# Optimization experiments

Hardware: AMD Instinct MI355X
Metric: run time of the kernel (lower is better)

Reference implementation:

```python
import jax, jax.numpy as jnp
import numpy as np

PARAM = 10.0
EPS = 1e-10

def delu(x):
    # delu_feature_map: param*relu(x) + (exp(param*min(x,0)) - 1) + 1
    return PARAM * jax.nn.relu(x) + jnp.expm1(PARAM * jnp.minimum(x, 0.0)) + 1.0

def conv1x1(x, w, b):
    # x: (B,C,H,W), w: (O,C), b: (O,)
    return jnp.einsum('oc,bchw->bohw', w, x) + b[None, :, None, None]

def conv3x3(x, w, b):
    # x: (B,C,H,W), w: (O,C,3,3)
    y = jax.lax.conv_general_dilated(x, w, window_strides=(1, 1), padding='SAME',
                                     dimension_numbers=('NCHW', 'OIHW', 'NCHW'))
    return y + b[None, :, None, None]

def setup_inputs() -> dict:
    key = jax.random.key(0)
    B, C, H, W = 4, 256, 128, 128
    ks = jax.random.split(key, 20)
    s = 0.05
    d = {
        'x1': jax.random.normal(ks[0], (B, C, H, W), jnp.float32),
        'x2': jax.random.normal(ks[1], (B, C, H, W), jnp.float32),
        'wq1': jax.random.normal(ks[2], (C, C), jnp.float32) * s,
        'bq1': jax.random.normal(ks[3], (C,), jnp.float32) * s,
        'wk1': jax.random.normal(ks[4], (C, C), jnp.float32) * s,
        'bk1': jax.random.normal(ks[5], (C,), jnp.float32) * s,
        'wv1': jax.random.normal(ks[6], (C, C), jnp.float32) * s,
        'bv1': jax.random.normal(ks[7], (C,), jnp.float32) * s,
        'wq2': jax.random.normal(ks[8], (C, C), jnp.float32) * s,
        'bq2': jax.random.normal(ks[9], (C,), jnp.float32) * s,
        'wk2': jax.random.normal(ks[10], (C, C), jnp.float32) * s,
        'bk2': jax.random.normal(ks[11], (C,), jnp.float32) * s,
        'wv2': jax.random.normal(ks[12], (C, C), jnp.float32) * s,
        'bv2': jax.random.normal(ks[13], (C,), jnp.float32) * s,
        'wd1': jax.random.normal(ks[14], (C, C), jnp.float32) * s,
        'bd1': jax.random.normal(ks[15], (C,), jnp.float32) * s,
        'wd3': jax.random.normal(ks[16], (C, C, 3, 3), jnp.float32) * s,
        'bd3': jax.random.normal(ks[17], (C,), jnp.float32) * s,
        'gamma1': jax.random.normal(ks[18], (1,), jnp.float32) * 0.5,
        'gamma2': jax.random.normal(ks[19], (1,), jnp.float32) * 0.5,
    }
    return d

def reference(x1, x2, wq1, bq1, wk1, bk1, wv1, bv1, wq2, bq2, wk2, bk2,
              wv2, bv2, wd1, bd1, wd3, bd3, gamma1, gamma2):
    B, C, H, W = x1.shape
    N = H * W
    # QKV projections (1x1 convs), flattened to (B,C,N). delu is elementwise,
    # so applying it on (B,C,N) equals the permute/delu/permute in torch.
    q1 = delu(conv1x1(x1, wq1, bq1).reshape(B, C, N))
    k1 = delu(conv1x1(x1, wk1, bk1).reshape(B, C, N))
    v1 = conv1x1(x1, wv1, bv1).reshape(B, C, N)
    q2 = delu(conv1x1(x2, wq2, bq2).reshape(B, C, N))
    k2 = delu(conv1x1(x2, wk2, bk2).reshape(B, C, N))
    v2 = conv1x1(x2, wv2, bv2).reshape(B, C, N)

    # energy: (B,C,C) cross-kernel matrices
    energy1 = jnp.einsum('bmn,bcn->bmc', q1, k2)
    energy2 = jnp.einsum('bmn,bcn->bmc', q2, k1)

    KV1 = k1 * v1  # (B,C,N)
    KV2 = k2 * v2

    # norm: 1 / (sum_{m,c} energy[b,m,c] * k[b,c,n] + eps) -> (B,N)
    esum1 = energy1.sum(axis=1)  # (B,C)
    esum2 = energy2.sum(axis=1)
    norm1 = 1.0 / (jnp.einsum('bc,bcn->bn', esum1, k2) + EPS)
    norm2 = 1.0 / (jnp.einsum('bc,bcn->bn', esum2, k1) + EPS)

    # einsum('bmc,bcn,bn->bcn') factorizes: sum over m hits only energy
    att1 = (esum1[:, :, None] * KV1 * norm1[:, None, :]).reshape(B, C, H, W)
    att2 = (esum2[:, :, None] * KV2 * norm2[:, None, :]).reshape(B, C, H, W)

    out1 = att1 + conv1x1(x1, wd1, bd1) + conv3x3(x1, wd3, bd3)
    out2 = att2 + conv1x1(x2, wd1, bd1) + conv3x3(x2, wd3, bd3)
    out1 = x1 + gamma1[0] * out1
    out2 = x2 + gamma2[0] * out2
    return (out1, out2)
```

## Files before the change

### kernel.cpp

```cpp
#include <hip/hip_runtime.h>
#include <stdint.h>

#define Bn 4
#define Cn 256
#define Hn 128
#define Wn 128
#define Nn 16384
#define EPSn 1e-10f

typedef unsigned short u16;
typedef __attribute__((ext_vector_type(8))) short short8;
typedef __attribute__((ext_vector_type(4))) short short4v;
typedef __attribute__((ext_vector_type(4))) float f32x4;

#define GLOAD_LDS16(g, l)                                                        \
    __builtin_amdgcn_global_load_lds(                                            \
        (const __attribute__((address_space(1))) unsigned int*)(const void*)(g), \
        (__attribute__((address_space(3))) unsigned int*)(void*)(l), 16, 0, 0)

#define MFMA16(a, b, c) __builtin_amdgcn_mfma_f32_16x16x32_bf16(a, b, c, 0, 0, 0)

__device__ __forceinline__ float bf2f(u16 u) {
    union { float f; uint32_t i; } v; v.i = ((uint32_t)u) << 16; return v.f;
}
__device__ __forceinline__ u16 f2bf(float f) {
    union { float f; uint32_t i; } v; v.f = f;
    uint32_t r = v.i + 0x7FFFu + ((v.i >> 16) & 1u);
    return (u16)(r >> 16);
}
__device__ __forceinline__ float delu_f(float x) {
    return x >= 0.f ? fmaf(10.f, x, 1.f) : __expf(10.f * x);
}

__global__ void prep_kernel(const float* __restrict__ wq1, const float* __restrict__ wk1,
                            const float* __restrict__ wv1,
                            const float* __restrict__ wq2, const float* __restrict__ wk2,
                            const float* __restrict__ wv2,
                            const float* __restrict__ wd1, const float* __restrict__ wd3,
                            const float* __restrict__ bd1, const float* __restrict__ bd3,
                            const float* __restrict__ gamma1, const float* __restrict__ gamma2,
                            u16* __restrict__ wq1p, u16* __restrict__ wk1p, u16* __restrict__ wv1p,
                            u16* __restrict__ wq2p, u16* __restrict__ wk2p, u16* __restrict__ wv2p,
                            u16* __restrict__ wallp1, u16* __restrict__ wallp2,
                            float* __restrict__ bfused)
{
    int idx = blockIdx.x * 256 + threadIdx.x;
    int o = idx >> 8, c = idx & 255;
    if (idx < 256) bfused[idx] = bd1[idx] + bd3[idx];
    int s = o >> 6, mf = (o >> 4) & 3, lr = o & 15;
    int kc = c >> 5, lk = (c >> 3) & 3, j = c & 7;
    int poff = ((kc * 4 + s) * 4 + mf) * 512 + (lk * 16 + lr) * 8 + j;
    wq1p[poff] = f2bf(wq1[idx]);
    wk1p[poff] = f2bf(wk1[idx]);
    wv1p[poff] = f2bf(wv1[idx]);
    wq2p[poff] = f2bf(wq2[idx]);
    wk2p[poff] = f2bf(wk2[idx]);
    wv2p[poff] = f2bf(wv2[idx]);
    float wd1v = wd1[idx];
    float inv1 = 1.f / gamma1[0];
    float inv2 = 1.f / gamma2[0];
    float diag = (o == c) ? 1.f : 0.f;
    #pragma unroll
    for (int tap = 0; tap < 9; ++tap) {
        float w = wd3[idx * 9 + tap] + (tap == 4 ? wd1v : 0.f);
        wallp1[tap * 65536 + poff] = f2bf(w + (tap == 4 ? diag * inv1 : 0.f));
        wallp2[tap * 65536 + poff] = f2bf(w + (tap == 4 ? diag * inv2 : 0.f));
    }
}

__global__ void transpose_kernel(const float* __restrict__ x, u16* __restrict__ xT)
{
    __shared__ __align__(16) u16 tl[64][72];
    int t = threadIdx.x;
    int n0 = blockIdx.x * 64, c0 = blockIdx.y * 64, b = blockIdx.z;
    int cl = t >> 4, nl = (t & 15) * 4;
    #pragma unroll
    for (int pc = 0; pc < 4; ++pc) {
        int c = pc * 16 + cl;
        float4 v = *(const float4*)&x[((size_t)(b * Cn + c0 + c)) * Nn + n0 + nl];
        tl[nl + 0][c] = f2bf(v.x);
        tl[nl + 1][c] = f2bf(v.y);
        tl[nl + 2][c] = f2bf(v.z);
        tl[nl + 3][c] = f2bf(v.w);
    }
    __syncthreads();
    #pragma unroll
    for (int ps = 0; ps < 2; ++ps) {
        int id = ps * 256 + t;
        int nr = id >> 3, cc = (id & 7) * 8;
        short8 v = *(const short8*)&tl[nr][cc];
        *(short8*)&xT[((size_t)(b * Nn + n0 + nr)) * 256 + c0 + cc] = v;
    }
}

__global__ __launch_bounds__(256, 2) void qk_kernel(
    const u16* __restrict__ xT,
    const u16* __restrict__ wqp, const u16* __restrict__ wkp,
    const float* __restrict__ bq, const float* __restrict__ bk,
    u16* __restrict__ kout, float* __restrict__ qsum)
{
    __shared__ __align__(16) u16 Bt[2 * 4096];
    int t = threadIdx.x;
    int nb = blockIdx.x, mb = blockIdx.y, b = blockIdx.z;
    int lane = t & 63, wid = t >> 6;
    int wm = wid >> 1, wn = wid & 1;
    int lr = lane & 15, lk = lane >> 4;
    int s = mb * 2 + wm;

    f32x4 zf = {0.f, 0.f, 0.f, 0.f};
    f32x4 accq[4][4], acck[4][4];
    #pragma unroll
    for (int i = 0; i < 4; ++i)
        #pragma unroll
        for (int j = 0; j < 4; ++j) { accq[i][j] = zf; acck[i][j] = zf; }

    int colp = lane >> 2, chp = (lane & 3) * 8;
    auto STAGE = [&](int bufi, int kc) {
        #pragma unroll
        for (int i = 0; i < 2; ++i) {
            int col0 = (wid * 2 + i) * 16;
            const u16* g = xT + ((size_t)(b * Nn + nb * 128 + col0 + colp)) * 256 + kc * 32 + chp;
            GLOAD_LDS16(g, &Bt[bufi * 4096 + col0 * 32]);
        }
    };

    STAGE(0, 0);
    __syncthreads();

    for (int kc = 0; kc < 8; ++kc) {
        int cur = kc & 1;
        int abase = ((kc * 4 + s) * 4) * 512 + lane * 8;
        short8 aq[4], ak[4];
        #pragma unroll
        for (int mf = 0; mf < 4; ++mf) {
            aq[mf] = *(const short8*)&wqp[abase + mf * 512];
            ak[mf] = *(const short8*)&wkp[abase + mf * 512];
        }
        if (kc < 7) STAGE(cur ^ 1, kc + 1);
        short8 bf[4];
        #pragma unroll
        for (int nf = 0; nf < 4; ++nf)
            bf[nf] = *(const short8*)&Bt[cur * 4096 + (wn * 64 + nf * 16 + lr) * 32 + lk * 8];
        __builtin_amdgcn_s_setprio(1);
        #pragma unroll
        for (int mf = 0; mf < 4; ++mf) {
            #pragma unroll
            for (int nf = 0; nf < 4; ++nf) {
                accq[mf][nf] = MFMA16(aq[mf], bf[nf], accq[mf][nf]);
                acck[mf][nf] = MFMA16(ak[mf], bf[nf], acck[mf][nf]);
            }
        }
        __builtin_amdgcn_s_setprio(0);
        __syncthreads();
    }

    float qs[4] = {0.f, 0.f, 0.f, 0.f};
    #pragma unroll
    for (int mf = 0; mf < 4; ++mf) {
        #pragma unroll
        for (int r = 0; r < 4; ++r) {
            int o = mb * 128 + wm * 64 + mf * 16 + lk * 4 + r;
            float bqv = bq[o], bkv = bk[o];
            #pragma unroll
            for (int nf = 0; nf < 4; ++nf) {
                int n = nb * 128 + wn * 64 + nf * 16 + lr;
                size_t idx = ((size_t)(b * Cn + o)) * Nn + n;
                float qv = delu_f(accq[mf][nf][r] + bqv);
                qs[nf] += qv;
                float kkv = delu_f(acck[mf][nf][r] + bkv);
                kout[idx] = f2bf(kkv);
            }
        }
    }
    #pragma unroll
    for (int nf = 0; nf < 4; ++nf) {
        float sgl = qs[nf];
        sgl += __shfl_xor(sgl, 16);
        sgl += __shfl_xor(sgl, 32);
        if (lk == 0)
            atomicAdd(&qsum[b * Nn + nb * 128 + wn * 64 + nf * 16 + lr], sgl);
    }
}

__global__ __launch_bounds__(256) void v_kernel(
    const u16* __restrict__ xT, const u16* __restrict__ wvp,
    const float* __restrict__ bv, u16* __restrict__ vout)
{
    __shared__ __align__(16) u16 Bt[2 * 4096];
    int t = threadIdx.x;
    int nb = blockIdx.x, mb = blockIdx.y, b = blockIdx.z;
    int lane = t & 63, wid = t >> 6;
    int wm = wid >> 1, wn = wid & 1;
    int lr = lane & 15, lk = lane >> 4;
    int s = mb * 2 + wm;

    f32x4 zf = {0.f, 0.f, 0.f, 0.f};
    f32x4 accv[4][4];
    #pragma unroll
    for (int i = 0; i < 4; ++i)
        #pragma unroll
        for (int j = 0; j < 4; ++j) accv[i][j] = zf;

    int colp = lane >> 2, chp = (lane & 3) * 8;
    auto STAGE = [&](int bufi, int kc) {
        #pragma unroll
        for (int i = 0; i < 2; ++i) {
            int col0 = (wid * 2 + i) * 16;
            const u16* g = xT + ((size_t)(b * Nn + nb * 128 + col0 + colp)) * 256 + kc * 32 + chp;
            GLOAD_LDS16(g, &Bt[bufi * 4096 + col0 * 32]);
        }
    };

    STAGE(0, 0);
    __syncthreads();

    for (int kc = 0; kc < 8; ++kc) {
        int cur = kc & 1;
        int abase = ((kc * 4 + s) * 4) * 512 + lane * 8;
        short8 av[4];
        #pragma unroll
        for (int mf = 0; mf < 4; ++mf)
            av[mf] = *(const short8*)&wvp[abase + mf * 512];
        if (kc < 7) STAGE(cur ^ 1, kc + 1);
        short8 bf[4];
        #pragma unroll
        for (int nf = 0; nf < 4; ++nf)
            bf[nf] = *(const short8*)&Bt[cur * 4096 + (wn * 64 + nf * 16 + lr) * 32 + lk * 8];
        __builtin_amdgcn_s_setprio(1);
        #pragma unroll
        for (int mf = 0; mf < 4; ++mf)
            #pragma unroll
            for (int nf = 0; nf < 4; ++nf)
                accv[mf][nf] = MFMA16(av[mf], bf[nf], accv[mf][nf]);
        __builtin_amdgcn_s_setprio(0);
        __syncthreads();
    }

    #pragma unroll
    for (int mf = 0; mf < 4; ++mf) {
        #pragma unroll
        for (int r = 0; r < 4; ++r) {
            int o = mb * 128 + wm * 64 + mf * 16 + lk * 4 + r;
            float bvv = bv[o];
            #pragma unroll
            for (int nf = 0; nf < 4; ++nf) {
                int n = nb * 128 + wn * 64 + nf * 16 + lr;
                vout[((size_t)(b * Cn + o)) * Nn + n] = f2bf(accv[mf][nf][r] + bvv);
            }
        }
    }
}

__global__ void esum_kernel(const u16* __restrict__ k, const float* __restrict__ qsum,
                            float* __restrict__ esum)
{
    int c = blockIdx.x, b = blockIdx.y, t = threadIdx.x;
    const u16* kr = k + ((size_t)(b * Cn + c)) * Nn;
    const float* qr = qsum + b * Nn;
    float s = 0.f;
    for (int i = t * 8; i < Nn; i += 2048) {
        short8 kv = *(const short8*)&kr[i];
        #pragma unroll
        for (int j = 0; j < 8; ++j) s = fmaf(bf2f((u16)kv[j]), qr[i + j], s);
    }
    #pragma unroll
    for (int m = 32; m; m >>= 1) s += __shfl_xor(s, m);
    __shared__ float red[4];
    if ((t & 63) == 0) red[t >> 6] = s;
    __syncthreads();
    if (t == 0) esum[b * Cn + c] = red[0] + red[1] + red[2] + red[3];
}

__global__ void norm_kernel(const u16* __restrict__ k, const float* __restrict__ esum,
                            float* __restrict__ nrm)
{
    __shared__ float es[256];
    int t = threadIdx.x, b = blockIdx.y;
    es[t] = esum[b * Cn + t];
    __syncthreads();
    int n = blockIdx.x * 256 + t;
    const u16* kb = k + (size_t)b * Cn * Nn + n;
    float a = 0.f;
    #pragma unroll 8
    for (int c = 0; c < 256; ++c)
        a = fmaf(es[c], bf2f(kb[(size_t)c * Nn]), a);
    nrm[b * Nn + n] = 1.f / (a + EPSn);
}

#define BSZ3 (3 * 130 * 32)

__global__ __launch_bounds__(256, 2) void conv_att_kernel(
    const u16* __restrict__ xT,
    const u16* __restrict__ wallp, const float* __restrict__ bfused,
    const u16* __restrict__ kk, const u16* __restrict__ vv,
    const float* __restrict__ esum, const float* __restrict__ nrm,
    const float* __restrict__ gamma, float* __restrict__ out)
{
    __shared__ __align__(16) u16 Bl[2 * BSZ3];
    int t = threadIdx.x;
    int lin = (blockIdx.z * 128 + blockIdx.y) * 2 + blockIdx.x;
    int wg = (lin & 7) * 128 + (lin >> 3);
    int mb = wg & 1, y = (wg >> 1) & 127, b = wg >> 8;
    int lane = t & 63, wid = t >> 6;
    int wm = wid >> 1, wp = wid & 1;
    int lr = lane & 15, lk = lane >> 4;
    int s = mb * 2 + wm;

    f32x4 zf = {0.f, 0.f, 0.f, 0.f};
    f32x4 acc[4][4];
    #pragma unroll
    for (int i = 0; i < 4; ++i)
        #pragma unroll
        for (int j = 0; j < 4; ++j) acc[i][j] = zf;

    if (t < 48) {
        int q = t & 3, slot = t >> 2;
        int buf = slot > 5 ? 1 : 0, r6 = slot - buf * 6;
        int row = r6 >> 1, pos = (r6 & 1) ? 129 : 0;
        short8 z = {0, 0, 0, 0, 0, 0, 0, 0};
        *(short8*)&Bl[buf * BSZ3 + (row * 130 + pos) * 32 + q * 8] = z;
    }

    int colp = lane >> 2, chp = (lane & 3) * 8;
    auto STAGE = [&](int bufi, int kc) {
        #pragma unroll
        for (int i = 0; i < 6; ++i) {
            int run = wid * 6 + i;
            int hy = run >> 3, sx = run & 7;
            int yy = y + hy - 1;
            int dst = bufi * BSZ3 + (hy * 130 + 1 + sx * 16) * 32;
            if (yy < 0 || yy >= Hn) {
                short8 z = {0, 0, 0, 0, 0, 0, 0, 0};
                *(short8*)&Bl[dst + lane * 8] = z;
            } else {
                const u16* g = xT + ((size_t)(b * Nn + yy * Wn + sx * 16 + colp)) * 256
                                  + kc * 32 + chp;
                GLOAD_LDS16(g, &Bl[dst]);
            }
        }
    };

    STAGE(0, 0);
    __syncthreads();

    for (int kc = 0; kc < 8; ++kc) {
        int cur = kc & 1;
        int abase = ((kc * 4 + s) * 4) * 512 + lane * 8;
        short8 af[9][4];
        #pragma unroll
        for (int tap = 0; tap < 9; ++tap)
            #pragma unroll
            for (int mf = 0; mf < 4; ++mf)
                af[tap][mf] = *(const short8*)&wallp[tap * 65536 + abase + mf * 512];
        if (kc < 7) STAGE(cur ^ 1, kc + 1);
        int cb = cur * BSZ3;
        #pragma unroll
        for (int dy = 0; dy < 3; ++dy) {
            #pragma unroll
            for (int dx = 0; dx < 3; ++dx) {
                int tap = dy * 3 + dx;
                short8 bf[4];
                #pragma unroll
                for (int nf = 0; nf < 4; ++nf)
                    bf[nf] = *(const short8*)&Bl[cb + (dy * 130 + wp * 64 + nf * 16 + lr + dx) * 32 + lk * 8];
                __builtin_amdgcn_s_setprio(1);
                #pragma unroll
                for (int mf = 0; mf < 4; ++mf) {
                    acc[mf][0] = MFMA16(af[tap][mf], bf[0], acc[mf][0]);
                    acc[mf][1] = MFMA16(af[tap][mf], bf[1], acc[mf][1]);
                    acc[mf][2] = MFMA16(af[tap][mf], bf[2], acc[mf][2]);
                    acc[mf][3] = MFMA16(af[tap][mf], bf[3], acc[mf][3]);
                }
                __builtin_amdgcn_s_setprio(0);
            }
        }
        __syncthreads();
    }

    float g = gamma[0];
    int nbase = y * Wn + wp * 64;
    float nr4[4];
    #pragma unroll
    for (int nf = 0; nf < 4; ++nf)
        nr4[nf] = nrm[b * Nn + nbase + nf * 16 + lr];
    #pragma unroll
    for (int mf = 0; mf < 4; ++mf) {
        #pragma unroll
        for (int r = 0; r < 4; ++r) {
            int o = mb * 128 + wm * 64 + mf * 16 + lk * 4 + r;
            float es_o = esum[b * Cn + o];
            float bf_o = bfused[o];
            size_t rowbase = ((size_t)(b * Cn + o)) * Nn + nbase;
            #pragma unroll
            for (int nf = 0; nf < 4; ++nf) {
                size_t idx = rowbase + nf * 16 + lr;
                float att = es_o * bf2f(kk[idx]) * bf2f(vv[idx]) * nr4[nf];
                out[idx] = g * (acc[mf][nf][r] + bf_o + att);
            }
        }
    }
}

extern "C" void kernel_launch(void* const* d_in, const int* in_sizes, int n_in,
                              void* d_out, int out_size, void* d_ws, size_t ws_size,
                              hipStream_t stream)
{
    const float* x1  = (const float*)d_in[0];
    const float* x2  = (const float*)d_in[1];
    const float* wq1 = (const float*)d_in[2];
    const float* bq1 = (const float*)d_in[3];
    const float* wk1 = (const float*)d_in[4];
    const float* bk1 = (const float*)d_in[5];
    const float* wv1 = (const float*)d_in[6];
    const float* bv1 = (const float*)d_in[7];
    const float* wq2 = (const float*)d_in[8];
    const float* bq2 = (const float*)d_in[9];
    const float* wk2 = (const float*)d_in[10];
    const float* bk2 = (const float*)d_in[11];
    const float* wv2 = (const float*)d_in[12];
    const float* bv2 = (const float*)d_in[13];
    const float* wd1 = (const float*)d_in[14];
    const float* bd1 = (const float*)d_in[15];
    const float* wd3 = (const float*)d_in[16];
    const float* bd3 = (const float*)d_in[17];
    const float* gamma1 = (const float*)d_in[18];
    const float* gamma2 = (const float*)d_in[19];

    char* ws = (char*)d_ws;
    size_t off = 0;
    auto alloc = [&](size_t bytes) { char* p = ws + off; off += (bytes + 255) & ~(size_t)255; return p; };

    u16* xT1    = (u16*)alloc((size_t)Bn * Nn * Cn * 2);
    u16* xT2    = (u16*)alloc((size_t)Bn * Nn * Cn * 2);
    u16* k1     = (u16*)alloc((size_t)Bn * Cn * Nn * 2);
    u16* k2     = (u16*)alloc((size_t)Bn * Cn * Nn * 2);
    u16* v2     = (u16*)alloc((size_t)Bn * Cn * Nn * 2);
    u16* wallp1 = (u16*)alloc((size_t)9 * 65536 * 2);
    u16* wallp2 = (u16*)alloc((size_t)9 * 65536 * 2);
    u16* wq1p   = (u16*)alloc(65536 * 2);
    u16* wk1p   = (u16*)alloc(65536 * 2);
    u16* wv1p   = (u16*)alloc(65536 * 2);
    u16* wq2p   = (u16*)alloc(65536 * 2);
    u16* wk2p   = (u16*)alloc(65536 * 2);
    u16* wv2p   = (u16*)alloc(65536 * 2);
    float* qsum1 = (float*)alloc(Bn * Nn * 4);
    float* qsum2 = (float*)alloc(Bn * Nn * 4);
    float* esum1 = (float*)alloc(Bn * Cn * 4);
    float* esum2 = (float*)alloc(Bn * Cn * 4);
    float* norm1 = (float*)alloc(Bn * Nn * 4);
    float* norm2 = (float*)alloc(Bn * Nn * 4);
    float* bfused = (float*)alloc(Cn * 4);

    float* out1 = (float*)d_out;
    float* out2 = out1 + (size_t)Bn * Cn * Nn;
    u16* v1 = (u16*)out2;

    hipMemsetAsync(qsum1, 0, Bn * Nn * 4, stream);
    hipMemsetAsync(qsum2, 0, Bn * Nn * 4, stream);

    prep_kernel<<<dim3(256), dim3(256), 0, stream>>>(wq1, wk1, wv1, wq2, wk2, wv2, wd1, wd3,
                                                     bd1, bd3, gamma1, gamma2,
                                                     wq1p, wk1p, wv1p, wq2p, wk2p, wv2p,
                                                     wallp1, wallp2, bfused);
    transpose_kernel<<<dim3(256, 4, 4), 256, 0, stream>>>(x1, xT1);
    transpose_kernel<<<dim3(256, 4, 4), 256, 0, stream>>>(x2, xT2);
    qk_kernel<<<dim3(128, 2, 4), 256, 0, stream>>>(xT1, wq1p, wk1p, bq1, bk1, k1, qsum1);
    qk_kernel<<<dim3(128, 2, 4), 256, 0, stream>>>(xT2, wq2p, wk2p, bq2, bk2, k2, qsum2);
    v_kernel<<<dim3(128, 2, 4), 256, 0, stream>>>(xT1, wv1p, bv1, v1);
    v_kernel<<<dim3(128, 2, 4), 256, 0, stream>>>(xT2, wv2p, bv2, v2);
    esum_kernel<<<dim3(256, 4), 256, 0, stream>>>(k2, qsum1, esum1);
    esum_kernel<<<dim3(256, 4), 256, 0, stream>>>(k1, qsum2, esum2);
    norm_kernel<<<dim3(64, 4), 256, 0, stream>>>(k2, esum1, norm1);
    norm_kernel<<<dim3(64, 4), 256, 0, stream>>>(k1, esum2, norm2);
    conv_att_kernel<<<dim3(2, 128, 4), 256, 0, stream>>>(xT1, wallp1, bfused, k1, v1,
                                                         esum1, norm1, gamma1, out1);
    conv_att_kernel<<<dim3(2, 128, 4), 256, 0, stream>>>(xT2, wallp2, bfused, k2, v2,
                                                         esum2, norm2, gamma2, out2);
}
```

Baseline: 392.1 us.

## Tile the 3x3 conv over four output rows per block, streaming weights per tap

The fused conv+attention kernel now has each 512-thread block compute four output rows. It stages a 6-row halo of the input in LDS instead of 3 rows per single output row, and each wave covers 128 pixels rather than 64. This cuts redundant halo loads and raises the MFMA work done per loaded weight and B fragment. Weight fragments are loaded through a rolling 3-tap register buffer instead of holding all 9 taps, which frees registers for the larger accumulator tile. The trade-off is a larger LDS footprint and a smaller grid with fewer resident waves per CU, which leaves less room to hide latency.

```diff
diff --git a/kernel.cpp b/kernel.cpp
--- a/kernel.cpp
+++ b/kernel.cpp
@@ -287,38 +287,37 @@
     nrm[b * Nn + n] = 1.f / (a + EPSn);
 }
 
-#define BSZ3 (3 * 130 * 32)
-
-__global__ __launch_bounds__(256, 2) void conv_att_kernel(
+#define BSZ6 (6 * 130 * 32)
+
+__global__ __launch_bounds__(512, 2) void conv_att_kernel(
     const u16* __restrict__ xT,
     const u16* __restrict__ wallp, const float* __restrict__ bfused,
     const u16* __restrict__ kk, const u16* __restrict__ vv,
     const float* __restrict__ esum, const float* __restrict__ nrm,
     const float* __restrict__ gamma, float* __restrict__ out)
 {
-    __shared__ __align__(16) u16 Bl[2 * BSZ3];
+    __shared__ __align__(16) u16 Bl[2 * BSZ6];
     int t = threadIdx.x;
-    int lin = (blockIdx.z * 128 + blockIdx.y) * 2 + blockIdx.x;
-    int wg = (lin & 7) * 128 + (lin >> 3);
-    int mb = wg & 1, y = (wg >> 1) & 127, b = wg >> 8;
+    int lin = (blockIdx.z * 32 + blockIdx.y) * 2 + blockIdx.x;
+    int mb = lin & 1, b = (lin >> 1) & 3, ys = lin >> 3;
+    int ybase = ys * 4;
     int lane = t & 63, wid = t >> 6;
-    int wm = wid >> 1, wp = wid & 1;
+    int wm = wid & 1, wy = wid >> 1;
     int lr = lane & 15, lk = lane >> 4;
     int s = mb * 2 + wm;
 
     f32x4 zf = {0.f, 0.f, 0.f, 0.f};
-    f32x4 acc[4][4];
+    f32x4 acc[4][8];
     #pragma unroll
     for (int i = 0; i < 4; ++i)
         #pragma unroll
-        for (int j = 0; j < 4; ++j) acc[i][j] = zf;
-
-    if (t < 48) {
-        int q = t & 3, slot = t >> 2;
-        int buf = slot > 5 ? 1 : 0, r6 = slot - buf * 6;
-        int row = r6 >> 1, pos = (r6 & 1) ? 129 : 0;
+        for (int j = 0; j < 8; ++j) acc[i][j] = zf;
+
+    if (t < 96) {
+        int buf = t / 48, r = t % 48;
+        int row = r >> 3, pos = ((r >> 2) & 1) ? 129 : 0, q = r & 3;
         short8 z = {0, 0, 0, 0, 0, 0, 0, 0};
-        *(short8*)&Bl[buf * BSZ3 + (row * 130 + pos) * 32 + q * 8] = z;
+        *(short8*)&Bl[buf * BSZ6 + (row * 130 + pos) * 32 + q * 8] = z;
     }
 
     int colp = lane >> 2, chp = (lane & 3) * 8;
@@ -327,8 +326,8 @@
         for (int i = 0; i < 6; ++i) {
             int run = wid * 6 + i;
             int hy = run >> 3, sx = run & 7;
-            int yy = y + hy - 1;
-            int dst = bufi * BSZ3 + (hy * 130 + 1 + sx * 16) * 32;
+            int yy = ybase + hy - 1;
+            int dst = bufi * BSZ6 + (hy * 130 + 1 + sx * 16) * 32;
             if (yy < 0 || yy >= Hn) {
                 short8 z = {0, 0, 0, 0, 0, 0, 0, 0};
                 *(short8*)&Bl[dst + lane * 8] = z;
@@ -346,43 +345,47 @@
     for (int kc = 0; kc < 8; ++kc) {
         int cur = kc & 1;
         int abase = ((kc * 4 + s) * 4) * 512 + lane * 8;
-        short8 af[9][4];
-        #pragma unroll
-        for (int tap = 0; tap < 9; ++tap)
-            #pragma unroll
-            for (int mf = 0; mf < 4; ++mf)
-                af[tap][mf] = *(const short8*)&wallp[tap * 65536 + abase + mf * 512];
+        short8 af[3][4];
+        #pragma unroll
+        for (int mf = 0; mf < 4; ++mf)
+            af[0][mf] = *(const short8*)&wallp[0 * 65536 + abase + mf * 512];
+        #pragma unroll
+        for (int mf = 0; mf < 4; ++mf)
+            af[1][mf] = *(const short8*)&wallp[1 * 65536 + abase + mf * 512];
         if (kc < 7) STAGE(cur ^ 1, kc + 1);
-        int cb = cur * BSZ3;
-        #pragma unroll
-        for (int dy = 0; dy < 3; ++dy) {
-            #pragma unroll
-            for (int dx = 0; dx < 3; ++dx) {
-                int tap = dy * 3 + dx;
-                short8 bf[4];
+        int cb = cur * BSZ6;
+        #pragma unroll
+        for (int tap = 0; tap < 9; ++tap) {
+            if (tap < 7) {
                 #pragma unroll
-                for (int nf = 0; nf < 4; ++nf)
-                    bf[nf] = *(const short8*)&Bl[cb + (dy * 130 + wp * 64 + nf * 16 + lr + dx) * 32 + lk * 8];
-                __builtin_amdgcn_s_setprio(1);
+                for (int mf = 0; mf < 4; ++mf)
+                    af[(tap + 2) % 3][mf] =
+                        *(const short8*)&wallp[(tap + 2) * 65536 + abase + mf * 512];
+            }
+            int dy = tap / 3, dx = tap % 3;
+            short8 bf[8];
+            #pragma unroll
+            for (int nf = 0; nf < 8; ++nf)
+                bf[nf] = *(const short8*)&Bl[cb + ((wy + dy) * 130 + nf * 16 + lr + dx) * 32 + lk * 8];
+            __builtin_amdgcn_s_setprio(1);
+            #pragma unroll
+            for (int mf = 0; mf < 4; ++mf) {
                 #pragma unroll
-                for (int mf = 0; mf < 4; ++mf) {
-                    acc[mf][0] = MFMA16(af[tap][mf], bf[0], acc[mf][0]);
-                    acc[mf][1] = MFMA16(af[tap][mf], bf[1], acc[mf][1]);
-                    acc[mf][2] = MFMA16(af[tap][mf], bf[2], acc[mf][2]);
-                    acc[mf][3] = MFMA16(af[tap][mf], bf[3], acc[mf][3]);
-                }
-                __builtin_amdgcn_s_setprio(0);
-            }
+                for (int nf = 0; nf < 8; ++nf)
+                    acc[mf][nf] = MFMA16(af[tap % 3][mf], bf[nf], acc[mf][nf]);
+            }
+            __builtin_amdgcn_s_setprio(0);
         }
         __syncthreads();
     }
 
     float g = gamma[0];
-    int nbase = y * Wn + wp * 64;
-    float nr4[4];
-    #pragma unroll
-    for (int nf = 0; nf < 4; ++nf)
-        nr4[nf] = nrm[b * Nn + nbase + nf * 16 + lr];
+    int y = ybase + wy;
+    int nbase = y * Wn;
+    float nr8[8];
+    #pragma unroll
+    for (int nf = 0; nf < 8; ++nf)
+        nr8[nf] = nrm[b * Nn + nbase + nf * 16 + lr];
     #pragma unroll
     for (int mf = 0; mf < 4; ++mf) {
         #pragma unroll
@@ -392,9 +395,9 @@
             float bf_o = bfused[o];
             size_t rowbase = ((size_t)(b * Cn + o)) * Nn + nbase;
             #pragma unroll
-            for (int nf = 0; nf < 4; ++nf) {
+            for (int nf = 0; nf < 8; ++nf) {
                 size_t idx = rowbase + nf * 16 + lr;
-                float att = es_o * bf2f(kk[idx]) * bf2f(vv[idx]) * nr4[nf];
+                float att = es_o * bf2f(kk[idx]) * bf2f(vv[idx]) * nr8[nf];
                 out[idx] = g * (acc[mf][nf][r] + bf_o + att);
             }
         }
@@ -472,8 +475,8 @@
     esum_kernel<<<dim3(256, 4), 256, 0, stream>>>(k1, qsum2, esum2);
     norm_kernel<<<dim3(64, 4), 256, 0, stream>>>(k2, esum1, norm1);
     norm_kernel<<<dim3(64, 4), 256, 0, stream>>>(k1, esum2, norm2);
-    conv_att_kernel<<<dim3(2, 128, 4), 256, 0, stream>>>(xT1, wallp1, bfused, k1, v1,
-                                                         esum1, norm1, gamma1, out1);
-    conv_att_kernel<<<dim3(2, 128, 4), 256, 0, stream>>>(xT2, wallp2, bfused, k2, v2,
-                                                         esum2, norm2, gamma2, out2);
-}
+    conv_att_kernel<<<dim3(2, 32, 4), 512, 0, stream>>>(xT1, wallp1, bfused, k1, v1,
+                                                        esum1, norm1, gamma1, out1);
+    conv_att_kernel<<<dim3(2, 32, 4), 512, 0, stream>>>(xT2, wallp2, bfused, k2, v2,
+                                                        esum2, norm2, gamma2, out2);
+}
```

New measurement: 375.8 us. 1.04x faster.

## Retile 3x3 conv into 2x64 pixel patches with halo edges and higher occupancy

Applied to the files above, without the earlier changes.

Changes each workgroup's spatial tile in the fused conv3x3+attention kernel from one full 128-pixel row to a 2-row by 64-column patch. The LDS halo buffer shrinks to 4x66 pixels and the left/right halo columns are loaded by a new EDGE routine. Launch bounds rise to 4 blocks per CU. Weight fragments are now loaded per tap inside the loop instead of preloading all 36 fragments up front, which cuts register pressure to allow the higher occupancy. In exchange, each block's halo is proportionally larger and weight loads are interleaved with the MFMAs, and the workgroup-to-tile mapping changes cache locality.

```diff
diff --git a/kernel.cpp b/kernel.cpp
--- a/kernel.cpp
+++ b/kernel.cpp
@@ -287,22 +287,23 @@
     nrm[b * Nn + n] = 1.f / (a + EPSn);
 }
 
-#define BSZ3 (3 * 130 * 32)
-
-__global__ __launch_bounds__(256, 2) void conv_att_kernel(
+#define BSZ4 (4 * 66 * 32)
+
+__global__ __launch_bounds__(256, 4) void conv_att_kernel(
     const u16* __restrict__ xT,
     const u16* __restrict__ wallp, const float* __restrict__ bfused,
     const u16* __restrict__ kk, const u16* __restrict__ vv,
     const float* __restrict__ esum, const float* __restrict__ nrm,
     const float* __restrict__ gamma, float* __restrict__ out)
 {
-    __shared__ __align__(16) u16 Bl[2 * BSZ3];
+    __shared__ __align__(16) u16 Bl[2 * BSZ4];
     int t = threadIdx.x;
     int lin = (blockIdx.z * 128 + blockIdx.y) * 2 + blockIdx.x;
-    int wg = (lin & 7) * 128 + (lin >> 3);
-    int mb = wg & 1, y = (wg >> 1) & 127, b = wg >> 8;
+    int mb = lin & 1, b = (lin >> 1) & 3, inner = lin >> 3;
+    int xs = inner & 1, ys = inner >> 1;
+    int ybase = ys * 2, x0 = xs * 64;
     int lane = t & 63, wid = t >> 6;
-    int wm = wid >> 1, wp = wid & 1;
+    int wm = wid & 1, wy = wid >> 1;
     int lr = lane & 15, lk = lane >> 4;
     int s = mb * 2 + wm;
 
@@ -313,72 +314,73 @@
         #pragma unroll
         for (int j = 0; j < 4; ++j) acc[i][j] = zf;
 
-    if (t < 48) {
-        int q = t & 3, slot = t >> 2;
-        int buf = slot > 5 ? 1 : 0, r6 = slot - buf * 6;
-        int row = r6 >> 1, pos = (r6 & 1) ? 129 : 0;
-        short8 z = {0, 0, 0, 0, 0, 0, 0, 0};
-        *(short8*)&Bl[buf * BSZ3 + (row * 130 + pos) * 32 + q * 8] = z;
-    }
-
     int colp = lane >> 2, chp = (lane & 3) * 8;
     auto STAGE = [&](int bufi, int kc) {
         #pragma unroll
-        for (int i = 0; i < 6; ++i) {
-            int run = wid * 6 + i;
-            int hy = run >> 3, sx = run & 7;
-            int yy = y + hy - 1;
-            int dst = bufi * BSZ3 + (hy * 130 + 1 + sx * 16) * 32;
+        for (int i = 0; i < 4; ++i) {
+            int run = wid * 4 + i;
+            int hy = run >> 2, seg = run & 3;
+            int yy = ybase + hy - 1;
+            int dst = bufi * BSZ4 + (hy * 66 + 1 + seg * 16) * 32;
             if (yy < 0 || yy >= Hn) {
                 short8 z = {0, 0, 0, 0, 0, 0, 0, 0};
                 *(short8*)&Bl[dst + lane * 8] = z;
             } else {
-                const u16* g = xT + ((size_t)(b * Nn + yy * Wn + sx * 16 + colp)) * 256
+                const u16* g = xT + ((size_t)(b * Nn + yy * Wn + x0 + seg * 16 + colp)) * 256
                                   + kc * 32 + chp;
                 GLOAD_LDS16(g, &Bl[dst]);
             }
         }
     };
+    auto EDGE = [&](int bufi, int kc) {
+        if (t < 32) {
+            int row = t >> 3, edge = (t >> 2) & 1, chq = t & 3;
+            int yy = ybase + row - 1;
+            int pxg = x0 + (edge ? 64 : -1);
+            short8 v = {0, 0, 0, 0, 0, 0, 0, 0};
+            if (yy >= 0 && yy < Hn && pxg >= 0 && pxg < Wn)
+                v = *(const short8*)&xT[((size_t)(b * Nn + yy * Wn + pxg)) * 256 + kc * 32 + chq * 8];
+            *(short8*)&Bl[bufi * BSZ4 + (row * 66 + (edge ? 65 : 0)) * 32 + chq * 8] = v;
+        }
+    };
 
     STAGE(0, 0);
+    EDGE(0, 0);
     __syncthreads();
 
     for (int kc = 0; kc < 8; ++kc) {
         int cur = kc & 1;
+        if (kc < 7) { STAGE(cur ^ 1, kc + 1); EDGE(cur ^ 1, kc + 1); }
+        int cb = cur * BSZ4;
         int abase = ((kc * 4 + s) * 4) * 512 + lane * 8;
-        short8 af[9][4];
-        #pragma unroll
-        for (int tap = 0; tap < 9; ++tap)
-            #pragma unroll
-            for (int mf = 0; mf < 4; ++mf)
-                af[tap][mf] = *(const short8*)&wallp[tap * 65536 + abase + mf * 512];
-        if (kc < 7) STAGE(cur ^ 1, kc + 1);
-        int cb = cur * BSZ3;
-        #pragma unroll
-        for (int dy = 0; dy < 3; ++dy) {
-            #pragma unroll
-            for (int dx = 0; dx < 3; ++dx) {
-                int tap = dy * 3 + dx;
-                short8 bf[4];
-                #pragma unroll
-                for (int nf = 0; nf < 4; ++nf)
-                    bf[nf] = *(const short8*)&Bl[cb + (dy * 130 + wp * 64 + nf * 16 + lr + dx) * 32 + lk * 8];
-                __builtin_amdgcn_s_setprio(1);
-                #pragma unroll
-                for (int mf = 0; mf < 4; ++mf) {
-                    acc[mf][0] = MFMA16(af[tap][mf], bf[0], acc[mf][0]);
-                    acc[mf][1] = MFMA16(af[tap][mf], bf[1], acc[mf][1]);
-                    acc[mf][2] = MFMA16(af[tap][mf], bf[2], acc[mf][2]);
-                    acc[mf][3] = MFMA16(af[tap][mf], bf[3], acc[mf][3]);
-                }
-                __builtin_amdgcn_s_setprio(0);
-            }
+        #pragma unroll
+        for (int tap = 0; tap < 9; ++tap) {
+            int dy = tap / 3, dx = tap % 3;
+            const u16* ap = wallp + tap * 65536 + abase;
+            short8 a0 = *(const short8*)&ap[0];
+            short8 a1 = *(const short8*)&ap[512];
+            short8 a2 = *(const short8*)&ap[1024];
+            short8 a3 = *(const short8*)&ap[1536];
+            short8 bf[4];
+            #pragma unroll
+            for (int nf = 0; nf < 4; ++nf)
+                bf[nf] = *(const short8*)&Bl[cb + ((wy + dy) * 66 + nf * 16 + lr + dx) * 32 + lk * 8];
+            __builtin_amdgcn_s_setprio(1);
+            #pragma unroll
+            for (int nf = 0; nf < 4; ++nf) {
+                acc[0][nf] = MFMA16(a0, bf[nf], acc[0][nf]);
+                acc[1][nf] = MFMA16(a1, bf[nf], acc[1][nf]);
+                acc[2][nf] = MFMA16(a2, bf[nf], acc[2][nf]);
+                acc[3][nf] = MFMA16(a3, bf[nf], acc[3][nf]);
+            }
+            __builtin_amdgcn_s_setprio(0);
         }
         __syncthreads();
     }
 
     float g = gamma[0];
-    int nbase = y * Wn + wp * 64;
+    int y = ybase + wy;
+    int nbase = y * Wn + x0;
     float nr4[4];
     #pragma unroll
     for (int nf = 0; nf < 4; ++nf)
```

New measurement: 391.5 us. No clear change (-0.1%).
